# Kernel tuning notes

Measured on AMD Instinct MI355X. Metric: run time of the kernel, lower is better.

Reference implementation:

```python
import jax, jax.numpy as jnp
import numpy as np

L, B, Q, P, D, H, F = 3, 256, 128, 16, 256, 16, 512
DK = D // H
SCALE = DK ** -0.5  # lsa=False -> constant scale
EPS = 1e-5


def _ln(x, g, b):
    m = jnp.mean(x, axis=-1, keepdims=True)
    v = jnp.mean(jnp.square(x - m), axis=-1, keepdims=True)
    return (x - m) * jax.lax.rsqrt(v + EPS) * g + b


def setup_inputs() -> dict:
    key = jax.random.key(0)
    ks = jax.random.split(key, 12)
    w = lambda k, shape: 0.02 * jax.random.normal(k, shape, dtype=jnp.float32)
    return {
        "x": jax.random.normal(ks[0], (B, Q, P), dtype=jnp.float32),
        "attn_bias": 0.1 * jax.random.normal(ks[1], (1, Q, Q), dtype=jnp.float32),
        "W_P": w(ks[2], (P, D)), "b_P": jnp.zeros((D,), jnp.float32),
        "W_pos": w(ks[3], (Q, D)),
        "Wq": w(ks[4], (L, D, D)), "bq": jnp.zeros((L, D), jnp.float32),
        "Wk": w(ks[5], (L, D, D)), "bk": jnp.zeros((L, D), jnp.float32),
        "Wv": w(ks[6], (L, D, D)), "bv": jnp.zeros((L, D), jnp.float32),
        "Wo": w(ks[7], (L, D, D)), "bo": jnp.zeros((L, D), jnp.float32),
        "ln1_g": jnp.ones((L, D), jnp.float32), "ln1_b": jnp.zeros((L, D), jnp.float32),
        "W1": w(ks[8], (L, D, F)), "b1": jnp.zeros((L, F), jnp.float32),
        "W2": w(ks[9], (L, F, D)), "b2": jnp.zeros((L, D), jnp.float32),
        "ln2_g": jnp.ones((L, D), jnp.float32), "ln2_b": jnp.zeros((L, D), jnp.float32),
    }


def _encoder(x, attn_bias, W_P, b_P, W_pos,
             Wq, bq, Wk, bk, Wv, bv, Wo, bo, ln1_g, ln1_b,
             W1, b1, W2, b2, ln2_g, ln2_b):
    # patch embedding + positional encoding (dropout=0, eval mode)
    z = x @ W_P + b_P + W_pos                      # [B, Q, D]
    bias = attn_bias[:, None]                      # [1, 1, Q, Q]

    def layer(carry, p):
        z, prev = carry
        (wq, bq_, wk, bk_, wv, bv_, wo, bo_, g1, be1, w1, b1_, w2, b2_, g2, be2) = p
        q = (z @ wq + bq_).reshape(B, Q, H, DK).transpose(0, 2, 1, 3)  # [B,H,Q,dk]
        k = (z @ wk + bk_).reshape(B, Q, H, DK).transpose(0, 2, 1, 3)
        v = (z @ wv + bv_).reshape(B, Q, H, DK).transpose(0, 2, 1, 3)
        # residual-attention + bias-augmented scores
        scores = jnp.einsum('bhqd,bhkd->bhqk', q, k) * SCALE + prev + bias
        attn = jax.nn.softmax(scores, axis=-1)
        o = jnp.einsum('bhqk,bhkd->bhqd', attn, v)
        o = o.transpose(0, 2, 1, 3).reshape(B, Q, D) @ wo + bo_
        z = _ln(z + o, g1, be1)                     # post-norm
        ffo = jax.nn.gelu(z @ w1 + b1_, approximate=False) @ w2 + b2_
        z = _ln(z + ffo, g2, be2)
        return (z, scores), None

    prev0 = jnp.zeros((B, H, Q, Q), z.dtype)        # prev=None == add zero
    params = (Wq, bq, Wk, bk, Wv, bv, Wo, bo, ln1_g, ln1_b,
              W1, b1, W2, b2, ln2_g, ln2_b)
    (z, _), _ = jax.lax.scan(layer, (z, prev0), params)
    return z


def reference(x, attn_bias, W_P, b_P, W_pos, Wq, bq, Wk, bk, Wv, bv, Wo, bo,
              ln1_g, ln1_b, W1, b1, W2, b2, ln2_g, ln2_b):
    return _encoder(x, attn_bias, W_P, b_P, W_pos, Wq, bq, Wk, bk, Wv, bv,
                    Wo, bo, ln1_g, ln1_b, W1, b1, W2, b2, ln2_g, ln2_b)
```

## Files before the change

### kernel.cpp

```cpp
#include <hip/hip_runtime.h>

#define DEV __device__ __forceinline__

typedef float          f32x4  __attribute__((ext_vector_type(4)));
typedef __bf16         bf16x8 __attribute__((ext_vector_type(8)));
typedef unsigned short u16x8  __attribute__((ext_vector_type(8)));

static constexpr int  Bq   = 256;
static constexpr int  Qs   = 128;
static constexpr int  Dm   = 256;
static constexpr int  Ff   = 512;
static constexpr int  ROWS = Bq * Qs;
static constexpr long QK_LSTR = (long)ROWS * 512;

DEV float b2f(unsigned short h) {
    unsigned int u = ((unsigned int)h) << 16;
    float f; __builtin_memcpy(&f, &u, 4); return f;
}
DEV unsigned short f2b(float f) {
    unsigned int u; __builtin_memcpy(&u, &f, 4);
    u += 0x7fffu + ((u >> 16) & 1u);
    return (unsigned short)(u >> 16);
}
DEV f32x4 mfma_bf16(u16x8 a, u16x8 b, f32x4 c) {
    return __builtin_amdgcn_mfma_f32_16x16x32_bf16(
        __builtin_bit_cast(bf16x8, a), __builtin_bit_cast(bf16x8, b), c, 0, 0, 0);
}
DEV void gl_lds16(const unsigned short* g, unsigned short* l) {
    __builtin_amdgcn_global_load_lds(
        (const __attribute__((address_space(1))) unsigned int*)g,
        (__attribute__((address_space(3))) unsigned int*)l, 16, 0, 0);
}

__global__ void k_embed(const float* __restrict__ x,
                        const float* __restrict__ WP,
                        const float* __restrict__ bP,
                        const float* __restrict__ Wpos,
                        unsigned short* __restrict__ zb) {
    int row = blockIdx.x;
    int d   = threadIdx.x;
    int q   = row & (Qs - 1);
    const float* xr = x + row * 16;
    float acc = bP[d] + Wpos[q * Dm + d];
#pragma unroll
    for (int p = 0; p < 16; p++) acc += xr[p] * WP[p * Dm + d];
    zb[(long)row * Dm + d] = f2b(acc);
}

static constexpr int S0 = 3 * 768 * 256;
static constexpr int S1 = 3 * 256 * 256;
static constexpr int S2 = 3 * 512 * 256;
static constexpr int S3 = 3 * 256 * 512;
static constexpr int S4 = 3 * 768;
static constexpr int S5 = 3 * 64 * 256;
static constexpr int PREP_TOT = S0 + S1 + S2 + S3 + S4 + S5;

__global__ void k_prep(const float* __restrict__ Wq, const float* __restrict__ Wk,
                       const float* __restrict__ Wv, const float* __restrict__ Wo,
                       const float* __restrict__ W1, const float* __restrict__ W2,
                       const float* __restrict__ bq, const float* __restrict__ bk,
                       const float* __restrict__ bv, const float* __restrict__ ab,
                       unsigned short* __restrict__ wTqkv, unsigned short* __restrict__ wTo,
                       unsigned short* __restrict__ wT1, unsigned short* __restrict__ wT2,
                       float* __restrict__ bqkv, float* __restrict__ pb) {
    int idx = blockIdx.x * 256 + threadIdx.x;
    if (idx < S0) {
        int l = idx / (768 * 256), r = idx % (768 * 256);
        int n = r / 256, k = r % 256;
        const float* W = (n < 256) ? Wq : (n < 512) ? Wk : Wv;
        float v = W[(long)l * 65536 + k * 256 + (n & 255)];
        if (n < 256) v *= 0.25f;
        wTqkv[idx] = f2b(v);
    } else if (idx < S0 + S1) {
        int j = idx - S0;
        int l = j / 65536, r = j % 65536, n = r / 256, k = r % 256;
        wTo[j] = f2b(Wo[(long)l * 65536 + k * 256 + n]);
    } else if (idx < S0 + S1 + S2) {
        int j = idx - S0 - S1;
        int l = j / (512 * 256), r = j % (512 * 256), n = r / 256, k = r % 256;
        wT1[j] = f2b(W1[(long)l * 131072 + k * 512 + n]);
    } else if (idx < S0 + S1 + S2 + S3) {
        int j = idx - S0 - S1 - S2;
        int l = j / (256 * 512), r = j % (256 * 512), n = r / 512, k = r % 512;
        wT2[j] = f2b(W2[(long)l * 131072 + k * 256 + n]);
    } else if (idx < S0 + S1 + S2 + S3 + S4) {
        int j = idx - S0 - S1 - S2 - S3;
        int l = j / 768, c = j % 768;
        float v = (c < 256) ? bq[l * 256 + c] * 0.25f
                : (c < 512) ? bk[l * 256 + c - 256]
                            : bv[l * 256 + c - 512];
        bqkv[j] = v;
    } else if (idx < PREP_TOT) {
        int j = idx - S0 - S1 - S2 - S3 - S4;
        int l = j / 16384, r = j % 16384;
        int u = r / 256, t = r % 256;
        int i = u >> 5, rr = (u >> 3) & 3, jj = u & 7;
        int wave = t >> 6, quad = (t >> 4) & 3, l16 = t & 15;
        int m = 32 * wave + 16 * i + 4 * quad + rr;
        int col = 16 * jj + l16;
        pb[j] = (float)(l + 1) * ab[m * 128 + col];
    }
}

template <int GELU, int MODE>
__global__ __launch_bounds__(256) void k_gemm(const unsigned short* __restrict__ A,
                                              const unsigned short* __restrict__ WT,
                                              const float* __restrict__ bias,
                                              unsigned short* __restrict__ outB,
                                              unsigned short* __restrict__ aux,
                                              int M, int N, int K) {
    __shared__ unsigned short smem[16384];
    unsigned short* As = smem;
    unsigned short* Bs = smem + 8192;
    const int tid  = threadIdx.x;
    const int wave = tid >> 6, lane = tid & 63, quad = lane >> 4, l16 = lane & 15;
    const int mq = wave >> 1, nq = wave & 1;
    const int m_blk = blockIdx.x * 128, n_blk = blockIdx.y * 128;
    const int c0 = tid, c1 = tid + 256;
    const int ra0 = c0 >> 2, ca0 = (c0 & 3) * 8;
    const int ra1 = c1 >> 2, ca1 = (c1 & 3) * 8;

    f32x4 acc[4][4] = {};

    for (int k0 = 0; k0 < K; k0 += 64) {
#pragma unroll
        for (int hh = 0; hh < 2; hh++) {
            int kk = k0 + hh * 32;
            gl_lds16(A  + (long)(m_blk + ra0) * K + kk + ca0, &As[hh * 4096 + c0 * 8]);
            gl_lds16(A  + (long)(m_blk + ra1) * K + kk + ca1, &As[hh * 4096 + c1 * 8]);
            gl_lds16(WT + (long)(n_blk + ra0) * K + kk + ca0, &Bs[hh * 4096 + c0 * 8]);
            gl_lds16(WT + (long)(n_blk + ra1) * K + kk + ca1, &Bs[hh * 4096 + c1 * 8]);
        }
        __syncthreads();
#pragma unroll
        for (int hh = 0; hh < 2; hh++) {
            u16x8 af[4], bf[4];
#pragma unroll
            for (int i = 0; i < 4; i++)
                af[i] = *(const u16x8*)&As[hh * 4096 + (64 * mq + 16 * i + l16) * 32 + quad * 8];
#pragma unroll
            for (int j = 0; j < 4; j++)
                bf[j] = *(const u16x8*)&Bs[hh * 4096 + (64 * nq + 16 * j + l16) * 32 + quad * 8];
#pragma unroll
            for (int i = 0; i < 4; i++)
#pragma unroll
                for (int j = 0; j < 4; j++)
                    acc[i][j] = mfma_bf16(af[i], bf[j], acc[i][j]);
        }
        __syncthreads();
    }

#pragma unroll
    for (int i = 0; i < 4; i++) {
        int rl = 64 * mq + 16 * i + quad * 4;
#pragma unroll
        for (int j = 0; j < 4; j++) {
            int cl = 64 * nq + 16 * j + l16;
            float bb = bias[n_blk + cl];
#pragma unroll
            for (int r = 0; r < 4; r++) {
                float v = acc[i][j][r] + bb;
                if (GELU) v = 0.5f * v * (1.0f + erff(v * 0.70710678118f));
                if (MODE == 0) smem[(rl + r) * 128 + cl] = f2b(v);
                if (MODE == 2) {
                    int g = 4 * nq + j;
                    smem[g * 2048 + (rl + r) * 16 + l16] = f2b(v);
                }
            }
        }
    }
    __syncthreads();
#pragma unroll
    for (int c = tid; c < 2048; c += 256) {
        u16x8 val = *(const u16x8*)&smem[c * 8];
        if (MODE == 0) {
            int row = c >> 4, seg = c & 15;
            *(u16x8*)&outB[(long)(m_blk + row) * N + n_blk + seg * 8] = val;
        }
        if (MODE == 2) {
            int g = c >> 8, w = c & 255;
            int n = n_blk + g * 16;
            if (n < 512) {
                int s = n >> 8, h = (n >> 4) & 15;
                *(u16x8*)&outB[((long)(((m_blk >> 7) * 16 + h) * 2 + s)) * 2048 + w * 8] = val;
            } else {
                int hh = (n - 512) >> 4;
                *(u16x8*)&aux[((long)hh * ROWS + m_blk) * 16 + w * 8] = val;
            }
        }
    }
}

template <int LAST, int AHM>
__global__ __launch_bounds__(256) void k_gemm_ln(const unsigned short* __restrict__ A,
                                                 const unsigned short* __restrict__ WT,
                                                 const float* __restrict__ bias,
                                                 const unsigned short* __restrict__ Zres,
                                                 const float* __restrict__ g,
                                                 const float* __restrict__ be,
                                                 unsigned short* __restrict__ zb,
                                                 float* __restrict__ outF,
                                                 int K) {
    __shared__ unsigned short smem[16384 + 2048 + 8192];
    unsigned short* Zs = smem;
    unsigned short* As = smem + 16384;
    unsigned short* Bs = smem + 16384 + 2048;
    float2* stats = (float2*)(smem + 16384);

    const int tid  = threadIdx.x;
    const int wave = tid >> 6, lane = tid & 63, quad = lane >> 4, l16 = lane & 15;
    const int m_blk = blockIdx.x * 64;

#pragma unroll
    for (int s = 0; s < 8; s++) {
        int c = tid + 256 * s;
        int zr = c >> 5, zc = (c & 31) * 8;
        gl_lds16(Zres + (long)(m_blk + zr) * 256 + zc, &Zs[c * 8]);
    }

    const int ca = (tid & 3) * 8, raA = tid >> 2;
    f32x4 acc[4][4] = {};

    for (int k0 = 0; k0 < K; k0 += 32) {
        if (AHM) {
            int k = k0 + ca;
            gl_lds16(A + ((long)(k >> 4) * ROWS + m_blk + raA) * 16 + (k & 15), &As[tid * 8]);
        } else {
            gl_lds16(A + (long)(m_blk + raA) * K + k0 + ca, &As[tid * 8]);
        }
#pragma unroll
        for (int s = 0; s < 4; s++) {
            int c = tid + 256 * s;
            int br = c >> 2, bc = (c & 3) * 8;
            gl_lds16(WT + (long)br * K + k0 + bc, &Bs[c * 8]);
        }
        __syncthreads();
        u16x8 af[4], bf[4];
#pragma unroll
        for (int i = 0; i < 4; i++)
            af[i] = *(const u16x8*)&As[(16 * i + l16) * 32 + quad * 8];
#pragma unroll
        for (int j = 0; j < 4; j++)
            bf[j] = *(const u16x8*)&Bs[(64 * wave + 16 * j + l16) * 32 + quad * 8];
#pragma unroll
        for (int i = 0; i < 4; i++)
#pragma unroll
            for (int j = 0; j < 4; j++)
                acc[i][j] = mfma_bf16(af[i], bf[j], acc[i][j]);
        __syncthreads();
    }

    float bb[4], gg[4], bt[4];
#pragma unroll
    for (int j = 0; j < 4; j++) {
        int col = 64 * wave + 16 * j + l16;
        bb[j] = bias[col]; gg[j] = g[col]; bt[j] = be[col];
    }
#pragma unroll
    for (int i = 0; i < 4; i++) {
#pragma unroll
        for (int r = 0; r < 4; r++) {
            int rloc = 16 * i + quad * 4 + r;
            float s1 = 0.f, s2 = 0.f;
#pragma unroll
            for (int j = 0; j < 4; j++) {
                int col = 64 * wave + 16 * j + l16;
                float v = acc[i][j][r] + bb[j] + b2f(Zs[rloc * 256 + col]);
                acc[i][j][r] = v;
                s1 += v; s2 += v * v;
            }
            for (int mk = 1; mk < 16; mk <<= 1) {
                s1 += __shfl_xor(s1, mk);
                s2 += __shfl_xor(s2, mk);
            }
            if (l16 == 0) stats[rloc * 4 + wave] = make_float2(s1, s2);
        }
    }
    __syncthreads();
#pragma unroll
    for (int i = 0; i < 4; i++) {
#pragma unroll
        for (int r = 0; r < 4; r++) {
            int rloc = 16 * i + quad * 4 + r;
            f32x4 p0 = *(const f32x4*)&stats[rloc * 4];
            f32x4 p1 = *(const f32x4*)&stats[rloc * 4 + 2];
            float S1 = p0[0] + p0[2] + p1[0] + p1[2];
            float S2 = p0[1] + p0[3] + p1[1] + p1[3];
            float mean = S1 * (1.0f / 256.0f);
            float var  = S2 * (1.0f / 256.0f) - mean * mean;
            float rstd = rsqrtf(var + 1e-5f);
            long grow = m_blk + rloc;
#pragma unroll
            for (int j = 0; j < 4; j++) {
                int col = 64 * wave + 16 * j + l16;
                float o = (acc[i][j][r] - mean) * rstd * gg[j] + bt[j];
                if (LAST) outF[grow * 256 + col] = o;
                else      zb[grow * 256 + col] = f2b(o);
            }
        }
    }
}

template <int L>
__global__ __launch_bounds__(256) void k_attn(const unsigned short* __restrict__ qkh,
                                              const unsigned short* __restrict__ vbuf,
                                              const float* __restrict__ pb,
                                              unsigned short* __restrict__ o_out) {
    __shared__ unsigned short vt[16 * 136];
    __shared__ unsigned short Ps[128 * 136];
    const int tid  = threadIdx.x;
    const int wave = tid >> 6, lane = tid & 63, quad = lane >> 4, l16 = lane & 15;
    const int b = blockIdx.x >> 4, h = blockIdx.x & 15;
    const int qrow = tid >> 1, half = tid & 1;

    u16x8 vv = *(const u16x8*)(vbuf + ((long)h * ROWS + b * Qs + qrow) * 16 + half * 8);
    const float* pbt = pb + (long)L * 16384 + tid;

    f32x4 accS[2][8] = {};
    u16x8 zero = {};

    constexpr int FULL = (L + 1) / 2;
    constexpr bool HALF = ((L + 1) & 1) != 0;

#pragma unroll
    for (int p = 0; p < FULL; p++) {
        const unsigned short* q0 = qkh + ((long)(((2 * p) * Bq + b) * 16 + h) * 2) * 2048;
        const unsigned short* q1 = qkh + ((long)(((2 * p + 1) * Bq + b) * 16 + h) * 2) * 2048;
        const unsigned short* qsel = (quad < 2) ? q0 : q1;
        const unsigned short* ksel = (quad < 2) ? (q0 + 2048) : (q1 + 2048);
        const int koff = (quad & 1) * 8;
        u16x8 af[2], bf8[8];
#pragma unroll
        for (int i = 0; i < 2; i++) {
            int m = 32 * wave + 16 * i + l16;
            af[i] = *(const u16x8*)(qsel + m * 16 + koff);
        }
#pragma unroll
        for (int j = 0; j < 8; j++) {
            int n = 16 * j + l16;
            bf8[j] = *(const u16x8*)(ksel + n * 16 + koff);
        }
#pragma unroll
        for (int i = 0; i < 2; i++)
#pragma unroll
            for (int j = 0; j < 8; j++)
                accS[i][j] = mfma_bf16(af[i], bf8[j], accS[i][j]);
    }
    if (HALF) {
        const unsigned short* qt = qkh + ((long)((L * Bq + b) * 16 + h) * 2) * 2048;
        const unsigned short* kt = qt + 2048;
        u16x8 af[2], bf8[8];
#pragma unroll
        for (int i = 0; i < 2; i++) {
            int m = 32 * wave + 16 * i + l16;
            af[i] = (quad < 2) ? *(const u16x8*)(qt + m * 16 + quad * 8) : zero;
        }
#pragma unroll
        for (int j = 0; j < 8; j++) {
            int n = 16 * j + l16;
            bf8[j] = (quad < 2) ? *(const u16x8*)(kt + n * 16 + quad * 8) : zero;
        }
#pragma unroll
        for (int i = 0; i < 2; i++)
#pragma unroll
            for (int j = 0; j < 8; j++)
                accS[i][j] = mfma_bf16(af[i], bf8[j], accS[i][j]);
    }

#pragma unroll
    for (int jj = 0; jj < 8; jj++) vt[(half * 8 + jj) * 136 + qrow] = vv[jj];

#pragma unroll
    for (int i = 0; i < 2; i++) {
#pragma unroll
        for (int r = 0; r < 4; r++) {
            int m = 32 * wave + 16 * i + quad * 4 + r;
#pragma unroll
            for (int j = 0; j < 8; j++) {
                int u = (i * 4 + r) * 8 + j;
                float s = accS[i][j][r] + pbt[u * 256];
                Ps[m * 136 + 16 * j + l16] = f2b(__expf(s));
            }
        }
    }
    __syncthreads();

    f32x4 accO[2] = {};
    f32x4 accR[2] = {};
    u16x8 ones;
#pragma unroll
    for (int jj = 0; jj < 8; jj++) ones[jj] = 0x3F80;
#pragma unroll
    for (int s = 0; s < 4; s++) {
        u16x8 bv = *(const u16x8*)&vt[l16 * 136 + s * 32 + quad * 8];
#pragma unroll
        for (int i = 0; i < 2; i++) {
            u16x8 ap = *(const u16x8*)&Ps[(32 * wave + 16 * i + l16) * 136 + s * 32 + quad * 8];
            accO[i] = mfma_bf16(ap, bv, accO[i]);
            accR[i] = mfma_bf16(ap, ones, accR[i]);
        }
    }
    __syncthreads();
#pragma unroll
    for (int i = 0; i < 2; i++)
#pragma unroll
        for (int r = 0; r < 4; r++) {
            int m = 32 * wave + 16 * i + quad * 4 + r;
            float inv = __builtin_amdgcn_rcpf(accR[i][r]);
            vt[m * 16 + l16] = f2b(accO[i][r] * inv);
        }
    __syncthreads();
    {
        unsigned short* obase = o_out + ((long)h * ROWS + b * Qs) * 16;
        *(u16x8*)&obase[tid * 8] = *(const u16x8*)&vt[tid * 8];
    }
}

extern "C" void kernel_launch(void* const* d_in, const int* in_sizes, int n_in,
                              void* d_out, int out_size, void* d_ws, size_t ws_size,
                              hipStream_t stream) {
    const float* x     = (const float*)d_in[0];
    const float* abias = (const float*)d_in[1];
    const float* WP    = (const float*)d_in[2];
    const float* bP    = (const float*)d_in[3];
    const float* Wpos  = (const float*)d_in[4];
    const float* Wq    = (const float*)d_in[5];
    const float* bqp   = (const float*)d_in[6];
    const float* Wk    = (const float*)d_in[7];
    const float* bkp   = (const float*)d_in[8];
    const float* Wv    = (const float*)d_in[9];
    const float* bvp   = (const float*)d_in[10];
    const float* Wo    = (const float*)d_in[11];
    const float* bo    = (const float*)d_in[12];
    const float* g1    = (const float*)d_in[13];
    const float* be1   = (const float*)d_in[14];
    const float* W1    = (const float*)d_in[15];
    const float* b1    = (const float*)d_in[16];
    const float* W2    = (const float*)d_in[17];
    const float* b2    = (const float*)d_in[18];
    const float* g2    = (const float*)d_in[19];
    const float* be2   = (const float*)d_in[20];
    (void)in_sizes; (void)n_in; (void)out_size; (void)ws_size;

    char* ws = (char*)d_ws;
    size_t off = 0;
    auto alloc = [&](size_t bytes) -> char* {
        char* p = ws + off; off += (bytes + 255) & ~(size_t)255; return p;
    };
    unsigned short* z_b   = (unsigned short*)alloc((size_t)ROWS * Dm * 2);
    unsigned short* qkh   = (unsigned short*)alloc((size_t)3 * ROWS * 512 * 2);
    unsigned short* v_cur = (unsigned short*)alloc((size_t)ROWS * Dm * 2);
    unsigned short* h1    = (unsigned short*)alloc((size_t)ROWS * Ff * 2);
    unsigned short* o_b   = h1;
    unsigned short* wTqkv = (unsigned short*)alloc((size_t)S0 * 2);
    unsigned short* wTo   = (unsigned short*)alloc((size_t)S1 * 2);
    unsigned short* wT1   = (unsigned short*)alloc((size_t)S2 * 2);
    unsigned short* wT2   = (unsigned short*)alloc((size_t)S3 * 2);
    float*          bqkv  = (float*)alloc((size_t)S4 * 4);
    float*          pb    = (float*)alloc((size_t)S5 * 4);

    k_prep<<<(PREP_TOT + 255) / 256, 256, 0, stream>>>(
        Wq, Wk, Wv, Wo, W1, W2, bqp, bkp, bvp, abias,
        wTqkv, wTo, wT1, wT2, bqkv, pb);
    k_embed<<<ROWS, 256, 0, stream>>>(x, WP, bP, Wpos, z_b);

    for (int l = 0; l < 3; l++) {
        k_gemm<0, 2><<<dim3(ROWS / 128, 6), 256, 0, stream>>>(
            z_b, wTqkv + (long)l * 768 * 256, bqkv + l * 768,
            qkh + (long)l * QK_LSTR, v_cur, ROWS, 768, 256);
        if (l == 0)      k_attn<0><<<Bq * 16, 256, 0, stream>>>(qkh, v_cur, pb, o_b);
        else if (l == 1) k_attn<1><<<Bq * 16, 256, 0, stream>>>(qkh, v_cur, pb, o_b);
        else             k_attn<2><<<Bq * 16, 256, 0, stream>>>(qkh, v_cur, pb, o_b);
        k_gemm_ln<0, 1><<<ROWS / 64, 256, 0, stream>>>(
            o_b, wTo + (long)l * 256 * 256, bo + l * 256, z_b,
            g1 + l * 256, be1 + l * 256, z_b, nullptr, 256);
        k_gemm<1, 0><<<dim3(ROWS / 128, 4), 256, 0, stream>>>(
            z_b, wT1 + (long)l * 512 * 256, b1 + l * 512, h1, nullptr, ROWS, 512, 256);
        if (l == 2)
            k_gemm_ln<1, 0><<<ROWS / 64, 256, 0, stream>>>(
                h1, wT2 + (long)l * 256 * 512, b2 + l * 256, z_b,
                g2 + l * 256, be2 + l * 256, nullptr, (float*)d_out, 512);
        else
            k_gemm_ln<0, 0><<<ROWS / 64, 256, 0, stream>>>(
                h1, wT2 + (long)l * 256 * 512, b2 + l * 256, z_b,
                g2 + l * 256, be2 + l * 256, z_b, nullptr, 512);
    }
}
```

Baseline: 550.5 us.

## Fuse FFN up-projection, GELU, down-projection and LayerNorm into one kernel

Replaces the separate W1 GEMM and W2 GEMM+LN launches with one k_ffn kernel. Each 64-row block keeps its z tile and a 256-wide hidden chunk in swizzled LDS, so the [ROWS,512] hidden activation never goes through global memory. The FFN weights are pre-packed into MFMA fragment order and read directly from global/L2 with no LDS staging. In exchange the kernel uses 64KB of LDS per block, which limits occupancy, and weight loads are not shared across waves through shared memory.

```diff
diff --git a/kernel.cpp b/kernel.cpp
--- a/kernel.cpp
+++ b/kernel.cpp
@@ -30,6 +30,9 @@
     __builtin_amdgcn_global_load_lds(
         (const __attribute__((address_space(1))) unsigned int*)g,
         (__attribute__((address_space(3))) unsigned int*)l, 16, 0, 0);
+}
+DEV int zadr(int row, int col) {
+    return row * 256 + ((((col >> 3) ^ (row & 7))) << 3) + (col & 7);
 }
 
 __global__ void k_embed(const float* __restrict__ x,
@@ -61,7 +64,7 @@
                        const float* __restrict__ bq, const float* __restrict__ bk,
                        const float* __restrict__ bv, const float* __restrict__ ab,
                        unsigned short* __restrict__ wTqkv, unsigned short* __restrict__ wTo,
-                       unsigned short* __restrict__ wT1, unsigned short* __restrict__ wT2,
+                       unsigned short* __restrict__ wp1, unsigned short* __restrict__ wp2,
                        float* __restrict__ bqkv, float* __restrict__ pb) {
     int idx = blockIdx.x * 256 + threadIdx.x;
     if (idx < S0) {
@@ -77,12 +80,18 @@
         wTo[j] = f2b(Wo[(long)l * 65536 + k * 256 + n]);
     } else if (idx < S0 + S1 + S2) {
         int j = idx - S0 - S1;
-        int l = j / (512 * 256), r = j % (512 * 256), n = r / 256, k = r % 256;
-        wT1[j] = f2b(W1[(long)l * 131072 + k * 512 + n]);
+        int l = j / 131072, r = j % 131072;
+        int tile = r >> 9, le = r & 511, lane = le >> 3, e = le & 7;
+        int ntile = tile >> 3, kk = tile & 7;
+        int n = ntile * 16 + (lane & 15), k = kk * 32 + (lane >> 4) * 8 + e;
+        wp1[j] = f2b(W1[(long)l * 131072 + k * 512 + n]);
     } else if (idx < S0 + S1 + S2 + S3) {
         int j = idx - S0 - S1 - S2;
-        int l = j / (256 * 512), r = j % (256 * 512), n = r / 512, k = r % 512;
-        wT2[j] = f2b(W2[(long)l * 131072 + k * 256 + n]);
+        int l = j / 131072, r = j % 131072;
+        int tile = r >> 9, le = r & 511, lane = le >> 3, e = le & 7;
+        int ntile = tile >> 4, kk = tile & 15;
+        int n = ntile * 16 + (lane & 15), k = kk * 32 + (lane >> 4) * 8 + e;
+        wp2[j] = f2b(W2[(long)l * 131072 + k * 256 + n]);
     } else if (idx < S0 + S1 + S2 + S3 + S4) {
         int j = idx - S0 - S1 - S2 - S3;
         int l = j / 768, c = j % 768;
@@ -299,6 +308,133 @@
             }
         }
     }
+}
+
+template <int LAST>
+__global__ __launch_bounds__(256, 2) void k_ffn(const unsigned short* __restrict__ zin,
+                                                const unsigned short* __restrict__ wp1,
+                                                const float* __restrict__ b1,
+                                                const unsigned short* __restrict__ wp2,
+                                                const float* __restrict__ b2,
+                                                const float* __restrict__ g2,
+                                                const float* __restrict__ be2,
+                                                unsigned short* __restrict__ zout,
+                                                float* __restrict__ outF) {
+    __shared__ unsigned short Zs[64 * 256];
+    __shared__ unsigned short Hs[64 * 256];
+    __shared__ float2 stats[64 * 4];
+
+    const int tid  = threadIdx.x;
+    const int wave = tid >> 6, lane = tid & 63, quad = (lane >> 4) & 3, l16 = lane & 15;
+    const int m_blk = blockIdx.x * 64;
+
+    {
+        int row = tid >> 2;
+#pragma unroll
+        for (int cc = 0; cc < 8; cc++) {
+            int c0 = (tid & 3) * 64 + cc * 8;
+            u16x8 v = *(const u16x8*)&zin[(long)(m_blk + row) * 256 + c0];
+            *(u16x8*)&Zs[zadr(row, c0)] = v;
+        }
+    }
+    __syncthreads();
+
+    f32x4 z2[4][4] = {};
+#pragma unroll 1
+    for (int c = 0; c < 2; c++) {
+        f32x4 a1[4][4] = {};
+#pragma unroll 2
+        for (int kk = 0; kk < 8; kk++) {
+            u16x8 af[4], bf[4];
+#pragma unroll
+            for (int i = 0; i < 4; i++)
+                af[i] = *(const u16x8*)&Zs[(16 * i + l16) * 256 + (((kk * 4 + quad) ^ (l16 & 7)) << 3)];
+#pragma unroll
+            for (int j = 0; j < 4; j++)
+                bf[j] = *(const u16x8*)&wp1[((long)(16 * c + 4 * wave + j) * 8 + kk) * 512 + lane * 8];
+#pragma unroll
+            for (int i = 0; i < 4; i++)
+#pragma unroll
+                for (int j = 0; j < 4; j++)
+                    a1[i][j] = mfma_bf16(af[i], bf[j], a1[i][j]);
+        }
+        __syncthreads();
+        float b1v[4];
+#pragma unroll
+        for (int j = 0; j < 4; j++) b1v[j] = b1[256 * c + 64 * wave + 16 * j + l16];
+#pragma unroll
+        for (int i = 0; i < 4; i++)
+#pragma unroll
+            for (int j = 0; j < 4; j++)
+#pragma unroll
+                for (int r = 0; r < 4; r++) {
+                    int row  = 16 * i + quad * 4 + r;
+                    int colh = 64 * wave + 16 * j + l16;
+                    float v = a1[i][j][r] + b1v[j];
+                    float gel = 0.5f * v * (1.0f + erff(v * 0.70710678118f));
+                    Hs[zadr(row, colh)] = f2b(gel);
+                }
+        __syncthreads();
+#pragma unroll 2
+        for (int kk = 0; kk < 8; kk++) {
+            u16x8 af[4], bf[4];
+#pragma unroll
+            for (int i = 0; i < 4; i++)
+                af[i] = *(const u16x8*)&Hs[(16 * i + l16) * 256 + (((kk * 4 + quad) ^ (l16 & 7)) << 3)];
+#pragma unroll
+            for (int j = 0; j < 4; j++)
+                bf[j] = *(const u16x8*)&wp2[((long)(4 * wave + j) * 16 + 8 * c + kk) * 512 + lane * 8];
+#pragma unroll
+            for (int i = 0; i < 4; i++)
+#pragma unroll
+                for (int j = 0; j < 4; j++)
+                    z2[i][j] = mfma_bf16(af[i], bf[j], z2[i][j]);
+        }
+    }
+
+    float b2v[4], gg[4], bb[4];
+#pragma unroll
+    for (int j = 0; j < 4; j++) {
+        int col = 64 * wave + 16 * j + l16;
+        b2v[j] = b2[col]; gg[j] = g2[col]; bb[j] = be2[col];
+    }
+#pragma unroll
+    for (int i = 0; i < 4; i++)
+#pragma unroll
+        for (int r = 0; r < 4; r++) {
+            int row = 16 * i + quad * 4 + r;
+            float s1 = 0.f, s2 = 0.f;
+#pragma unroll
+            for (int j = 0; j < 4; j++) {
+                int col = 64 * wave + 16 * j + l16;
+                float v = z2[i][j][r] + b2v[j] + b2f(Zs[zadr(row, col)]);
+                z2[i][j][r] = v; s1 += v; s2 += v * v;
+            }
+            for (int mk = 1; mk < 16; mk <<= 1) { s1 += __shfl_xor(s1, mk); s2 += __shfl_xor(s2, mk); }
+            if (l16 == 0) stats[row * 4 + wave] = make_float2(s1, s2);
+        }
+    __syncthreads();
+#pragma unroll
+    for (int i = 0; i < 4; i++)
+#pragma unroll
+        for (int r = 0; r < 4; r++) {
+            int row = 16 * i + quad * 4 + r;
+            f32x4 p0 = *(const f32x4*)&stats[row * 4];
+            f32x4 p1 = *(const f32x4*)&stats[row * 4 + 2];
+            float S1 = p0[0] + p0[2] + p1[0] + p1[2];
+            float S2 = p0[1] + p0[3] + p1[1] + p1[3];
+            float mean = S1 * (1.0f / 256.0f);
+            float var  = S2 * (1.0f / 256.0f) - mean * mean;
+            float rstd = rsqrtf(var + 1e-5f);
+            long grow = m_blk + row;
+#pragma unroll
+            for (int j = 0; j < 4; j++) {
+                int col = 64 * wave + 16 * j + l16;
+                float o = (z2[i][j][r] - mean) * rstd * gg[j] + bb[j];
+                if (LAST) outF[grow * 256 + col] = o;
+                else      zout[grow * 256 + col] = f2b(o);
+            }
+        }
 }
 
 template <int L>
@@ -450,18 +586,17 @@
     unsigned short* z_b   = (unsigned short*)alloc((size_t)ROWS * Dm * 2);
     unsigned short* qkh   = (unsigned short*)alloc((size_t)3 * ROWS * 512 * 2);
     unsigned short* v_cur = (unsigned short*)alloc((size_t)ROWS * Dm * 2);
-    unsigned short* h1    = (unsigned short*)alloc((size_t)ROWS * Ff * 2);
-    unsigned short* o_b   = h1;
+    unsigned short* o_b   = (unsigned short*)alloc((size_t)ROWS * Dm * 2);
     unsigned short* wTqkv = (unsigned short*)alloc((size_t)S0 * 2);
     unsigned short* wTo   = (unsigned short*)alloc((size_t)S1 * 2);
-    unsigned short* wT1   = (unsigned short*)alloc((size_t)S2 * 2);
-    unsigned short* wT2   = (unsigned short*)alloc((size_t)S3 * 2);
+    unsigned short* wp1   = (unsigned short*)alloc((size_t)S2 * 2);
+    unsigned short* wp2   = (unsigned short*)alloc((size_t)S3 * 2);
     float*          bqkv  = (float*)alloc((size_t)S4 * 4);
     float*          pb    = (float*)alloc((size_t)S5 * 4);
 
     k_prep<<<(PREP_TOT + 255) / 256, 256, 0, stream>>>(
         Wq, Wk, Wv, Wo, W1, W2, bqp, bkp, bvp, abias,
-        wTqkv, wTo, wT1, wT2, bqkv, pb);
+        wTqkv, wTo, wp1, wp2, bqkv, pb);
     k_embed<<<ROWS, 256, 0, stream>>>(x, WP, bP, Wpos, z_b);
 
     for (int l = 0; l < 3; l++) {
@@ -474,15 +609,15 @@
         k_gemm_ln<0, 1><<<ROWS / 64, 256, 0, stream>>>(
             o_b, wTo + (long)l * 256 * 256, bo + l * 256, z_b,
             g1 + l * 256, be1 + l * 256, z_b, nullptr, 256);
-        k_gemm<1, 0><<<dim3(ROWS / 128, 4), 256, 0, stream>>>(
-            z_b, wT1 + (long)l * 512 * 256, b1 + l * 512, h1, nullptr, ROWS, 512, 256);
         if (l == 2)
-            k_gemm_ln<1, 0><<<ROWS / 64, 256, 0, stream>>>(
-                h1, wT2 + (long)l * 256 * 512, b2 + l * 256, z_b,
-                g2 + l * 256, be2 + l * 256, nullptr, (float*)d_out, 512);
+            k_ffn<1><<<ROWS / 64, 256, 0, stream>>>(
+                z_b, wp1 + (long)l * 131072, b1 + l * 512,
+                wp2 + (long)l * 131072, b2 + l * 256,
+                g2 + l * 256, be2 + l * 256, nullptr, (float*)d_out);
         else
-            k_gemm_ln<0, 0><<<ROWS / 64, 256, 0, stream>>>(
-                h1, wT2 + (long)l * 256 * 512, b2 + l * 256, z_b,
-                g2 + l * 256, be2 + l * 256, z_b, nullptr, 512);
-    }
-}
+            k_ffn<0><<<ROWS / 64, 256, 0, stream>>>(
+                z_b, wp1 + (long)l * 131072, b1 + l * 512,
+                wp2 + (long)l * 131072, b2 + l * 256,
+                g2 + l * 256, be2 + l * 256, z_b, nullptr);
+    }
+}
```

Measured after the change: 500.3 us. -9.1%, faster.
